# Kernel optimization log

Hardware: AMD Instinct MI355X
Metric: run time of the kernel (lower is better)

Reference implementation:

```python
import jax, jax.numpy as jnp
import numpy as np

H = 256        # hidden_dim == num_features
C = 10         # num_classes
N = 100000     # nodes
E = 1600000    # edges
BN_EPS = 1e-5
NEG_SLOPE = 0.1


def _bn(h, gamma, beta):
    # training-mode BatchNorm1d over node dim, biased variance (torch semantics)
    mu = jnp.mean(h, axis=0)
    var = jnp.mean(jnp.square(h - mu), axis=0)
    return (h - mu) * jax.lax.rsqrt(var + BN_EPS) * gamma + beta


def setup_inputs() -> dict:
    key = jax.random.key(0)
    ks = jax.random.split(key, 12)
    s = 1.0 / np.sqrt(H)
    x = jax.random.normal(ks[0], (N, H), dtype=jnp.float32)
    edge_index = jax.random.randint(ks[1], (2, E), 0, N, dtype=jnp.int64)
    return {
        "x": x,
        "edge_index": edge_index,
        # GIN MLP: lin1 -> bn -> relu -> lin2
        "W1": jax.random.uniform(ks[2], (H, H), jnp.float32, -s, s),
        "b1": jnp.zeros((H,), jnp.float32),
        "g_mlp": jnp.ones((H,), jnp.float32),
        "be_mlp": jnp.zeros((H,), jnp.float32),
        "W2": jax.random.uniform(ks[3], (H, H), jnp.float32, -s, s),
        "b2": jnp.zeros((H,), jnp.float32),
        # bn4
        "g4": jnp.ones((H,), jnp.float32),
        "be4": jnp.zeros((H,), jnp.float32),
        # head
        "Wl1": jax.random.uniform(ks[4], (H, H // 2), jnp.float32, -s, s),
        "bl1": jnp.zeros((H // 2,), jnp.float32),
        "Wl3": jax.random.uniform(ks[5], (H // 2, C), jnp.float32, -s, s),
        "bl3": jnp.zeros((C,), jnp.float32),
    }


def reference(x, edge_index, W1, b1, g_mlp, be_mlp, W2, b2, g4, be4, Wl1, bl1, Wl3, bl3):
    lrelu = lambda h: jax.nn.leaky_relu(h, NEG_SLOPE)
    src, dst = edge_index[0], edge_index[1]
    # GINConv: sum-aggregate neighbor messages (source_to_target), eps=0
    agg = jax.ops.segment_sum(x[src], dst, num_segments=x.shape[0])  # [N,H]
    h = agg + x  # (1+eps)*x + sum
    # PyG MLP([H,H,H]): lin -> batch_norm -> relu -> lin (plain last)
    h = jax.nn.relu(_bn(h @ W1 + b1, g_mlp, be_mlp)) @ W2 + b2
    x1 = lrelu(h)                     # relu(conv1(...), 0.1); dropout p=0
    h = lrelu(x1)                     # relu(x1, 0.1)
    h = lrelu(_bn(h, g4, be4))        # relu(bn4(x), 0.1); dropout p=0
    h = x + 0.01 * h                  # residual with original features
    h = lrelu(h @ Wl1 + bl1)
    return h @ Wl3 + bl3              # [N, C]
```

## Files before the change

### kernel.cpp

```cpp
#include <hip/hip_runtime.h>

constexpr int NN = 100000;
constexpr int NE = 1600000;
constexpr int NBUCK = 782;
constexpr int CGRID = 98;

typedef __attribute__((ext_vector_type(4))) float  f32x4;
typedef __attribute__((ext_vector_type(2))) float  f32x2;
typedef __attribute__((ext_vector_type(8))) short  bf16x8;

__device__ __forceinline__ float bf2f(unsigned short u) {
  union { unsigned int i; float f; } c;
  c.i = ((unsigned int)u) << 16;
  return c.f;
}
__device__ __forceinline__ short f2bf(float f) {
  union { float f; unsigned int i; } c; c.f = f;
  unsigned int i = c.i + 0x7fffu + ((c.i >> 16) & 1u);
  return (short)(i >> 16);
}
__device__ __forceinline__ unsigned char f2fp8(float f) {
  int w = __builtin_amdgcn_cvt_pk_fp8_f32(f, 0.f, 0, false);
  return (unsigned char)(w & 0xff);
}
__device__ __forceinline__ void up4(int wv, float* f) {
  f32x2 a = __builtin_amdgcn_cvt_pk_f32_fp8(wv, false);
  f32x2 b = __builtin_amdgcn_cvt_pk_f32_fp8(wv, true);
  f[0] = a[0]; f[1] = a[1]; f[2] = b[0]; f[3] = b[1];
}

__device__ __forceinline__ void gload16(const void* g, void* l) {
  __builtin_amdgcn_global_load_lds(
      (const __attribute__((address_space(1))) unsigned int*)g,
      (__attribute__((address_space(3))) unsigned int*)l, 16, 0, 0);
}

__global__ void k_detect(const int* __restrict__ ew, int* __restrict__ flag,
                         float* __restrict__ zst) {
  __shared__ int bad;
  if (threadIdx.x == 0) bad = 0;
  for (int i = threadIdx.x; i < 1024; i += 256) zst[i] = 0.f;
  __syncthreads();
  int nz = 0;
  for (int i = threadIdx.x; i < 2048; i += 256) nz |= ew[2 * i + 1];
  if (nz) atomicOr(&bad, 1);
  __syncthreads();
  if (threadIdx.x == 0) *flag = (bad == 0) ? 1 : 0;
}

__global__ void k_cvtW(const float* __restrict__ W1, const float* __restrict__ W2,
                       const float* __restrict__ Wl1, const float* __restrict__ Wl3,
                       unsigned char* __restrict__ W1T8, unsigned char* __restrict__ W2T8,
                       short* __restrict__ Wl1T, short* __restrict__ Wl3T) {
  int b = blockIdx.x, t = threadIdx.x;
  if (b < 256)       W1T8[b * 256 + t]       = f2fp8(W1[t * 256 + b]);
  else if (b < 512){ int n = b - 256; W2T8[n * 256 + t] = f2fp8(W2[t * 256 + n]); }
  else if (b < 640){ int n = b - 512; Wl1T[n * 256 + t] = f2bf(Wl1[t * 128 + n]); }
  else {
    if (t < 128) {
#pragma unroll
      for (int c = 0; c < 16; ++c)
        Wl3T[c * 128 + t] = (c < 10) ? f2bf(Wl3[t * 10 + c]) : (short)0;
    }
  }
}

__global__ void k_cvtX(const float* __restrict__ x, void* __restrict__ xq) {
  int c = blockIdx.x * 256 + threadIdx.x;
  float4 a = ((const float4*)x)[2 * (size_t)c];
  float4 b = ((const float4*)x)[2 * (size_t)c + 1];
  int p0 = 0, p1 = 0;
  p0 = __builtin_amdgcn_cvt_pk_fp8_f32(a.x, a.y, p0, false);
  p0 = __builtin_amdgcn_cvt_pk_fp8_f32(a.z, a.w, p0, true);
  p1 = __builtin_amdgcn_cvt_pk_fp8_f32(b.x, b.y, p1, false);
  p1 = __builtin_amdgcn_cvt_pk_fp8_f32(b.z, b.w, p1, true);
  ((int2*)xq)[c] = make_int2(p0, p1);
}

__global__ __launch_bounds__(1024) void k_count(const int* __restrict__ ew,
                                                const int* __restrict__ flag,
                                                int* __restrict__ cntmat) {
  __shared__ int lcnt[NBUCK];
  int m64 = *flag;
  int t = threadIdx.x;
  for (int i = t; i < NBUCK; i += 1024) lcnt[i] = 0;
  __syncthreads();
  int base = blockIdx.x * 16384;
#pragma unroll
  for (int u = 0; u < 16; u++) {
    int e = base + u * 1024 + t;
    if (e < NE) {
      int d = m64 ? ew[2 * (NE + e)] : ew[NE + e];
      atomicAdd(&lcnt[d >> 7], 1);
    }
  }
  __syncthreads();
  for (int i = t; i < NBUCK; i += 1024) cntmat[blockIdx.x * NBUCK + i] = lcnt[i];
}

__global__ __launch_bounds__(1024) void k_colscan(int* __restrict__ cntmat,
                                                  int* __restrict__ bases,
                                                  int* __restrict__ off_) {
  __shared__ int tot[1024];
  int t = threadIdx.x;
  int sum = 0;
  if (t < NBUCK) {
    for (int g = 0; g < CGRID; g++) sum += cntmat[g * NBUCK + t];
    tot[t] = sum;
  }
  __syncthreads();
  int v = (t < NBUCK) ? sum : 0;
  for (int o = 1; o < 1024; o <<= 1) {
    int u = (t >= o && t < NBUCK) ? tot[t - o] : 0;
    __syncthreads();
    if (t < NBUCK) tot[t] += u;
    __syncthreads();
  }
  if (t < NBUCK) {
    int b = tot[t] - v;
    bases[t] = b;
    int run = b;
    for (int g = 0; g < CGRID; g++) {
      int c = cntmat[g * NBUCK + t];
      cntmat[g * NBUCK + t] = run;
      run += c;
    }
  }
  if (t == NBUCK) bases[NBUCK] = NE;
  if (t == NBUCK + 1) off_[NN] = NE;
}

__global__ __launch_bounds__(1024) void k_scatter(const int* __restrict__ ew,
                                                  const int* __restrict__ flag,
                                                  const int* __restrict__ cntmat,
                                                  int* __restrict__ pairs) {
  __shared__ int lcur[NBUCK];
  int m64 = *flag;
  int t = threadIdx.x;
  for (int i = t; i < NBUCK; i += 1024) lcur[i] = cntmat[blockIdx.x * NBUCK + i];
  __syncthreads();
  int base = blockIdx.x * 16384;
#pragma unroll
  for (int u = 0; u < 16; u++) {
    int e = base + u * 1024 + t;
    if (e < NE) {
      int d = m64 ? ew[2 * (NE + e)] : ew[NE + e];
      int s = m64 ? ew[2 * e] : ew[e];
      int slot = atomicAdd(&lcur[d >> 7], 1);
      pairs[slot] = s | ((d & 127) << 17);
    }
  }
}

__global__ __launch_bounds__(256) void k_bsort(const int* __restrict__ pairs,
                                               const int* __restrict__ bases,
                                               int* __restrict__ off_,
                                               int* __restrict__ csr) {
  __shared__ int lcnt[128], lofs[128], lcur[128];
  int b = blockIdx.x, t = threadIdx.x;
  int s0 = bases[b], s1 = bases[b + 1];
  if (t < 128) lcnt[t] = 0;
  __syncthreads();
  for (int j = s0 + t; j < s1; j += 256) atomicAdd(&lcnt[(pairs[j] >> 17) & 127], 1);
  __syncthreads();
  int v = (t < 128) ? lcnt[t] : 0;
  if (t < 128) lofs[t] = v;
  __syncthreads();
  for (int o = 1; o < 128; o <<= 1) {
    int u = (t >= o && t < 128) ? lofs[t - o] : 0;
    __syncthreads();
    if (t < 128) lofs[t] += u;
    __syncthreads();
  }
  if (t < 128) {
    int ex = lofs[t] - v;
    lcur[t] = ex;
    int node = b * 128 + t;
    if (node < NN) off_[node] = s0 + ex;
  }
  __syncthreads();
  for (int j = s0 + t; j < s1; j += 256) {
    int p = pairs[j];
    int slot = atomicAdd(&lcur[(p >> 17) & 127], 1);
    csr[s0 + slot] = p & 0x1FFFF;
  }
}

__global__ __launch_bounds__(256) void k_agg2(const void* __restrict__ xq,
                                              const int* __restrict__ off_,
                                              const int* __restrict__ csr,
                                              unsigned char* __restrict__ h0) {
  int node = blockIdx.x * 4 + (threadIdx.x >> 6);
  int lane = threadIdx.x & 63;
  const unsigned char* xb = (const unsigned char*)xq;
  size_t boff = (size_t)lane * 4;
  int s0 = off_[node], s1 = off_[node + 1];
  int sw = *(const int*)(xb + (size_t)node * 256 + boff);
  f32x2 slo = __builtin_amdgcn_cvt_pk_f32_fp8(sw, false);
  f32x2 shi = __builtin_amdgcn_cvt_pk_f32_fp8(sw, true);
  float a0 = slo[0], a1 = slo[1], a2 = shi[0], a3 = shi[1];
  int j = s0;
  while (j + 8 <= s1) {
    int idx[8];
#pragma unroll
    for (int u = 0; u < 8; u++) idx[u] = csr[j + u];
    int w[8];
#pragma unroll
    for (int u = 0; u < 8; u++) w[u] = *(const int*)(xb + (size_t)idx[u] * 256 + boff);
#pragma unroll
    for (int u = 0; u < 8; u++) {
      f32x2 lo = __builtin_amdgcn_cvt_pk_f32_fp8(w[u], false);
      f32x2 hi = __builtin_amdgcn_cvt_pk_f32_fp8(w[u], true);
      a0 += lo[0]; a1 += lo[1]; a2 += hi[0]; a3 += hi[1];
    }
    j += 8;
  }
  if (j + 4 <= s1) {
    int idx[4];
#pragma unroll
    for (int u = 0; u < 4; u++) idx[u] = csr[j + u];
    int w[4];
#pragma unroll
    for (int u = 0; u < 4; u++) w[u] = *(const int*)(xb + (size_t)idx[u] * 256 + boff);
#pragma unroll
    for (int u = 0; u < 4; u++) {
      f32x2 lo = __builtin_amdgcn_cvt_pk_f32_fp8(w[u], false);
      f32x2 hi = __builtin_amdgcn_cvt_pk_f32_fp8(w[u], true);
      a0 += lo[0]; a1 += lo[1]; a2 += hi[0]; a3 += hi[1];
    }
    j += 4;
  }
  for (; j < s1; j++) {
    int s = csr[j];
    int w = *(const int*)(xb + (size_t)s * 256 + boff);
    f32x2 lo = __builtin_amdgcn_cvt_pk_f32_fp8(w, false);
    f32x2 hi = __builtin_amdgcn_cvt_pk_f32_fp8(w, true);
    a0 += lo[0]; a1 += lo[1]; a2 += hi[0]; a3 += hi[1];
  }
  int o = 0;
  o = __builtin_amdgcn_cvt_pk_fp8_f32(a0, a1, o, false);
  o = __builtin_amdgcn_cvt_pk_fp8_f32(a2, a3, o, true);
  ((int*)h0)[(size_t)node * 64 + lane] = o;
}

template <int ACT, int TIN, int STATS>
__global__ __launch_bounds__(256, 2) void k_gemm8(
    const unsigned char* __restrict__ A, const unsigned char* __restrict__ BT,
    const float* __restrict__ bias, unsigned char* __restrict__ C, int M,
    const float* __restrict__ tsum, const float* __restrict__ tssq,
    const float* __restrict__ tg, const float* __restrict__ tbe,
    float* __restrict__ gsum, float* __restrict__ gssq) {
  __shared__ char smem[32768];
  __shared__ float lsc[256], lsh[256];
  __shared__ float lsum[128], lssq[128];
  int tid = threadIdx.x, lane = tid & 63, w = tid >> 6;
  if (TIN) {
    float mu = tsum[tid] / (float)M;
    float var = tssq[tid] / (float)M - mu * mu;
    float rs = rsqrtf(var + 1e-5f);
    float sc = tg[tid] * rs;
    lsc[tid] = sc; lsh[tid] = tbe[tid] - mu * sc;
  }
  if (STATS && tid < 128) { lsum[tid] = 0.f; lssq[tid] = 0.f; }
  int bm = blockIdx.x >> 1, bn = blockIdx.x & 1;
  int bm0 = bm * 128, bn0 = bn * 128;
  int wm = w >> 1, wn = w & 1;
  int lr = lane & 15, lg = lane >> 4;
  f32x4 acc[4][4] = {};
  __syncthreads();

  int4 stg[2];

#pragma unroll 1
  for (int it = 0; it < 4; ++it) {
    int b = it & 1;
    if (it == 0) {
      if (TIN) {
#pragma unroll
        for (int i = 0; i < 2; ++i) {
          int p = i * 256 + tid, unit = p >> 3, u = (p & 7) ^ (unit & 7);
          int srow = unit * 2 + (u >> 2), slot = u & 3;
          int grow = bm0 + srow; if (grow > M - 1) grow = M - 1;
          stg[i] = *(const int4*)(A + (size_t)grow * 256 + slot * 16);
        }
      } else {
#pragma unroll
        for (int q = 0; q < 2; ++q) {
          int wc = w * 2 + q;
          int p = wc * 64 + lane, unit = p >> 3, u = (p & 7) ^ (unit & 7);
          int srow = unit * 2 + (u >> 2), slot = u & 3;
          int grow = bm0 + srow; if (grow > M - 1) grow = M - 1;
          gload16(A + (size_t)grow * 256 + slot * 16, smem + wc * 1024);
        }
      }
#pragma unroll
      for (int q = 0; q < 2; ++q) {
        int wc = w * 2 + q;
        int p = wc * 64 + lane, unit = p >> 3, u = (p & 7) ^ (unit & 7);
        int srow = unit * 2 + (u >> 2), slot = u & 3;
        gload16(BT + (size_t)(bn0 + srow) * 256 + slot * 16, smem + 8192 + wc * 1024);
      }
      if (TIN) {
#pragma unroll
        for (int i = 0; i < 2; ++i) {
          int p = i * 256 + tid, unit = p >> 3, u = (p & 7) ^ (unit & 7);
          int slot = u & 3;
          int k0 = slot * 16;
          float f[16];
          up4(stg[i].x, f); up4(stg[i].y, f + 4); up4(stg[i].z, f + 8); up4(stg[i].w, f + 12);
#pragma unroll
          for (int jj = 0; jj < 16; ++jj) f[jj] = fmaxf(f[jj] * lsc[k0 + jj] + lsh[k0 + jj], 0.f);
          int w0 = 0, w1 = 0, w2 = 0, w3 = 0;
          w0 = __builtin_amdgcn_cvt_pk_fp8_f32(f[0], f[1], w0, false);
          w0 = __builtin_amdgcn_cvt_pk_fp8_f32(f[2], f[3], w0, true);
          w1 = __builtin_amdgcn_cvt_pk_fp8_f32(f[4], f[5], w1, false);
          w1 = __builtin_amdgcn_cvt_pk_fp8_f32(f[6], f[7], w1, true);
          w2 = __builtin_amdgcn_cvt_pk_fp8_f32(f[8], f[9], w2, false);
          w2 = __builtin_amdgcn_cvt_pk_fp8_f32(f[10], f[11], w2, true);
          w3 = __builtin_amdgcn_cvt_pk_fp8_f32(f[12], f[13], w3, false);
          w3 = __builtin_amdgcn_cvt_pk_fp8_f32(f[14], f[15], w3, true);
          *(int4*)(smem + p * 16) = make_int4(w0, w1, w2, w3);
        }
      }
      __syncthreads();
    }
    int ktn = (it + 1) * 64;
    if (it < 3) {
      char* nb = smem + (b ^ 1) * 16384;
      if (TIN) {
#pragma unroll
        for (int i = 0; i < 2; ++i) {
          int p = i * 256 + tid, unit = p >> 3, u = (p & 7) ^ (unit & 7);
          int srow = unit * 2 + (u >> 2), slot = u & 3;
          int grow = bm0 + srow; if (grow > M - 1) grow = M - 1;
          stg[i] = *(const int4*)(A + (size_t)grow * 256 + ktn + slot * 16);
        }
      } else {
#pragma unroll
        for (int q = 0; q < 2; ++q) {
          int wc = w * 2 + q;
          int p = wc * 64 + lane, unit = p >> 3, u = (p & 7) ^ (unit & 7);
          int srow = unit * 2 + (u >> 2), slot = u & 3;
          int grow = bm0 + srow; if (grow > M - 1) grow = M - 1;
          gload16(A + (size_t)grow * 256 + ktn + slot * 16, nb + wc * 1024);
        }
      }
#pragma unroll
      for (int q = 0; q < 2; ++q) {
        int wc = w * 2 + q;
        int p = wc * 64 + lane, unit = p >> 3, u = (p & 7) ^ (unit & 7);
        int srow = unit * 2 + (u >> 2), slot = u & 3;
        gload16(BT + (size_t)(bn0 + srow) * 256 + ktn + slot * 16, nb + 8192 + wc * 1024);
      }
    }
    const char* sa = smem + b * 16384;
    const char* sb = sa + 8192;
#pragma unroll
    for (int ks = 0; ks < 2; ++ks) {
      long af[4], bfr[4];
#pragma unroll
      for (int mi = 0; mi < 4; ++mi) {
        int row = wm * 64 + mi * 16 + lr;
        int unit = row >> 1;
        int u = ((row & 1) * 4 + ks * 2 + (lg >> 1)) ^ (unit & 7);
        af[mi] = *(const long*)(sa + unit * 128 + u * 16 + (lg & 1) * 8);
      }
#pragma unroll
      for (int ni = 0; ni < 4; ++ni) {
        int row = wn * 64 + ni * 16 + lr;
        int unit = row >> 1;
        int u = ((row & 1) * 4 + ks * 2 + (lg >> 1)) ^ (unit & 7);
        bfr[ni] = *(const long*)(sb + unit * 128 + u * 16 + (lg & 1) * 8);
      }
#pragma unroll
      for (int mi = 0; mi < 4; ++mi)
#pragma unroll
        for (int ni = 0; ni < 4; ++ni)
          acc[mi][ni] = __builtin_amdgcn_mfma_f32_16x16x32_fp8_fp8(af[mi], bfr[ni], acc[mi][ni], 0, 0, 0);
    }
    if (TIN && it < 3) {
      char* nb = smem + (b ^ 1) * 16384;
#pragma unroll
      for (int i = 0; i < 2; ++i) {
        int p = i * 256 + tid, unit = p >> 3, u = (p & 7) ^ (unit & 7);
        int slot = u & 3;
        int k0 = ktn + slot * 16;
        float f[16];
        up4(stg[i].x, f); up4(stg[i].y, f + 4); up4(stg[i].z, f + 8); up4(stg[i].w, f + 12);
#pragma unroll
        for (int jj = 0; jj < 16; ++jj) f[jj] = fmaxf(f[jj] * lsc[k0 + jj] + lsh[k0 + jj], 0.f);
        int w0 = 0, w1 = 0, w2 = 0, w3 = 0;
        w0 = __builtin_amdgcn_cvt_pk_fp8_f32(f[0], f[1], w0, false);
        w0 = __builtin_amdgcn_cvt_pk_fp8_f32(f[2], f[3], w0, true);
        w1 = __builtin_amdgcn_cvt_pk_fp8_f32(f[4], f[5], w1, false);
        w1 = __builtin_amdgcn_cvt_pk_fp8_f32(f[6], f[7], w1, true);
        w2 = __builtin_amdgcn_cvt_pk_fp8_f32(f[8], f[9], w2, false);
        w2 = __builtin_amdgcn_cvt_pk_fp8_f32(f[10], f[11], w2, true);
        w3 = __builtin_amdgcn_cvt_pk_fp8_f32(f[12], f[13], w3, false);
        w3 = __builtin_amdgcn_cvt_pk_fp8_f32(f[14], f[15], w3, true);
        *(int4*)(nb + p * 16) = make_int4(w0, w1, w2, w3);
      }
    }
    __syncthreads();
  }

  unsigned char* zs = (unsigned char*)smem;
#pragma unroll
  for (int ni = 0; ni < 4; ++ni) {
    int col = wn * 64 + ni * 16 + lr;
    float bv = bias[bn0 + col];
    float ps = 0.f, pq = 0.f;
#pragma unroll
    for (int mi = 0; mi < 4; ++mi) {
#pragma unroll
      for (int r = 0; r < 4; ++r) {
        int row = wm * 64 + mi * 16 + lg * 4 + r;
        float tv = acc[mi][ni][r] + bv;
        if (ACT == 1) tv = tv > 0.f ? tv : 0.01f * tv;
        if (STATS && (bm0 + row) < M) { ps += tv; pq += tv * tv; }
        zs[row * 144 + col] = f2fp8(tv);
      }
    }
    if (STATS) {
      ps += __shfl_xor(ps, 16); pq += __shfl_xor(pq, 16);
      ps += __shfl_xor(ps, 32); pq += __shfl_xor(pq, 32);
      if (lane < 16) {
        atomicAdd(&lsum[wn * 64 + ni * 16 + lane], ps);
        atomicAdd(&lssq[wn * 64 + ni * 16 + lane], pq);
      }
    }
  }
  __syncthreads();
  {
    int row = tid >> 1;
    int grow = bm0 + row;
    if (grow < M) {
#pragma unroll
      for (int i = 0; i < 4; ++i) {
        int cs = (tid & 1) * 64 + i * 16;
        int4 v = *(const int4*)(zs + row * 144 + cs);
        *(int4*)(C + (size_t)grow * 256 + bn0 + cs) = v;
      }
    }
  }
  if (STATS) {
    if (tid < 128) {
      atomicAdd(&gsum[bn0 + tid], lsum[tid]);
      atomicAdd(&gssq[bn0 + tid], lssq[tid]);
    }
  }
}

__global__ __launch_bounds__(256, 2) void k_head(const unsigned char* __restrict__ Vq,
                                                 const float* __restrict__ x,
                                                 const short* __restrict__ BT,
                                                 const float* __restrict__ bl1,
                                                 const short* __restrict__ wl3t,
                                                 const float* __restrict__ bl3,
                                                 const float* __restrict__ tsum,
                                                 const float* __restrict__ tssq,
                                                 const float* __restrict__ tg,
                                                 const float* __restrict__ tbe,
                                                 float* __restrict__ out, int M) {
  __shared__ char smem[65536];
  __shared__ float lsc[256], lsh[256];
  __shared__ short wl3s[2048];
  int tid = threadIdx.x;
  int lane = tid & 63, w = tid >> 6;
  {
    float mu = tsum[tid] / (float)M;
    float var = tssq[tid] / (float)M - mu * mu;
    float rs = rsqrtf(var + 1e-5f);
    float sc = tg[tid] * rs;
    lsc[tid] = sc; lsh[tid] = tbe[tid] - mu * sc;
  }
  {
    int p = w * 64 + lane;
    gload16(wl3t + (size_t)p * 8, (char*)wl3s + w * 1024);
  }
  int bm0 = blockIdx.x * 128;
  int wm = w >> 1, wn = w & 1;
  int lr = lane & 15, lg = lane >> 4;
  f32x4 acc[4][4] = {};
  __syncthreads();

  int2 stgv[4];
  float stgx[4][8];

#pragma unroll 1
  for (int it = 0; it < 4; ++it) {
    int b = it & 1;
    if (it == 0) {
#pragma unroll
      for (int i = 0; i < 4; ++i) {
        int p = tid + 256 * i, row = p >> 3, s = (p & 7) ^ (row & 7);
        int grow = bm0 + row; if (grow > M - 1) grow = M - 1;
        size_t base = (size_t)grow * 256 + s * 8;
        stgv[i] = *(const int2*)(Vq + base);
        *(float4*)&stgx[i][0] = *(const float4*)(x + base);
        *(float4*)&stgx[i][4] = *(const float4*)(x + base + 4);
      }
#pragma unroll
      for (int q = 0; q < 4; ++q) {
        int wc = w * 4 + q;
        int p = wc * 64 + lane, row = p >> 3, s = (p & 7) ^ (row & 7);
        gload16(BT + (size_t)row * 256 + s * 8, smem + 16384 + wc * 1024);
      }
#pragma unroll
      for (int i = 0; i < 4; ++i) {
        int p = tid + 256 * i, row = p >> 3, s = (p & 7) ^ (row & 7);
        int k0 = s * 8;
        float fv[8];
        up4(stgv[i].x, fv); up4(stgv[i].y, fv + 4);
        bf16x8 o;
#pragma unroll
        for (int jj = 0; jj < 8; ++jj) {
          float f = fv[jj] * lsc[k0 + jj] + lsh[k0 + jj];
          f = f > 0.f ? f : 0.1f * f;
          o[jj] = f2bf(stgx[i][jj] + 0.01f * f);
        }
        *(bf16x8*)(smem + p * 16) = o;
      }
      __syncthreads();
    }
    int ktn = (it + 1) * 64;
    if (it < 3) {
      char* nb = smem + (b ^ 1) * 32768;
#pragma unroll
      for (int i = 0; i < 4; ++i) {
        int p = tid + 256 * i, row = p >> 3, s = (p & 7) ^ (row & 7);
        int grow = bm0 + row; if (grow > M - 1) grow = M - 1;
        size_t base = (size_t)grow * 256 + ktn + s * 8;
        stgv[i] = *(const int2*)(Vq + base);
        *(float4*)&stgx[i][0] = *(const float4*)(x + base);
        *(float4*)&stgx[i][4] = *(const float4*)(x + base + 4);
      }
#pragma unroll
      for (int q = 0; q < 4; ++q) {
        int wc = w * 4 + q;
        int p = wc * 64 + lane, row = p >> 3, s = (p & 7) ^ (row & 7);
        gload16(BT + (size_t)row * 256 + ktn + s * 8, nb + 16384 + wc * 1024);
      }
    }
    const char* sa = smem + b * 32768;
    const char* sb = sa + 16384;
#pragma unroll
    for (int ks = 0; ks < 2; ++ks) {
      bf16x8 af[4], bfr[4];
#pragma unroll
      for (int mi = 0; mi < 4; ++mi) {
        int row = wm * 64 + mi * 16 + lr;
        int q = (lg + 4 * ks) ^ (row & 7);
        af[mi] = *(const bf16x8*)(sa + row * 128 + q * 16);
      }
#pragma unroll
      for (int ni = 0; ni < 4; ++ni) {
        int row = wn * 64 + ni * 16 + lr;
        int q = (lg + 4 * ks) ^ (row & 7);
        bfr[ni] = *(const bf16x8*)(sb + row * 128 + q * 16);
      }
#pragma unroll
      for (int mi = 0; mi < 4; ++mi)
#pragma unroll
        for (int ni = 0; ni < 4; ++ni)
          acc[mi][ni] = __builtin_amdgcn_mfma_f32_16x16x32_bf16(af[mi], bfr[ni], acc[mi][ni], 0, 0, 0);
    }
    if (it < 3) {
      char* nb = smem + (b ^ 1) * 32768;
#pragma unroll
      for (int i = 0; i < 4; ++i) {
        int p = tid + 256 * i, row = p >> 3, s = (p & 7) ^ (row & 7);
        int k0 = ktn + s * 8;
        float fv[8];
        up4(stgv[i].x, fv); up4(stgv[i].y, fv + 4);
        bf16x8 o;
#pragma unroll
        for (int jj = 0; jj < 8; ++jj) {
          float f = fv[jj] * lsc[k0 + jj] + lsh[k0 + jj];
          f = f > 0.f ? f : 0.1f * f;
          o[jj] = f2bf(stgx[i][jj] + 0.01f * f);
        }
        *(bf16x8*)(nb + p * 16) = o;
      }
    }
    __syncthreads();
  }

  short* zs = (short*)smem;
#pragma unroll
  for (int ni = 0; ni < 4; ++ni) {
    int col = wn * 64 + ni * 16 + lr;
    float bv = bl1[col];
#pragma unroll
    for (int mi = 0; mi < 4; ++mi) {
#pragma unroll
      for (int r = 0; r < 4; ++r) {
        int row = wm * 64 + mi * 16 + lg * 4 + r;
        float tv = acc[mi][ni][r] + bv;
        tv = tv > 0.f ? tv : 0.1f * tv;
        zs[row * 136 + col] = f2bf(tv);
      }
    }
  }
  __syncthreads();

  f32x4 acc2[2] = {};
#pragma unroll
  for (int kk = 0; kk < 4; ++kk) {
    bf16x8 bfr = *(const bf16x8*)((const char*)wl3s + lr * 256 + (kk * 4 + lg) * 16);
#pragma unroll
    for (int m = 0; m < 2; ++m) {
      int row = (w * 2 + m) * 16 + lr;
      bf16x8 af = *(const bf16x8*)((const char*)zs + row * 272 + (kk * 4 + lg) * 16);
      acc2[m] = __builtin_amdgcn_mfma_f32_16x16x32_bf16(af, bfr, acc2[m], 0, 0, 0);
    }
  }
  if (lr < 10) {
    float bv = bl3[lr];
#pragma unroll
    for (int m = 0; m < 2; ++m) {
#pragma unroll
      for (int r = 0; r < 4; ++r) {
        int row = (w * 2 + m) * 16 + lg * 4 + r;
        int grow = bm0 + row;
        if (grow < M) out[(size_t)grow * 10 + lr] = acc2[m][r] + bv;
      }
    }
  }
}

extern "C" void kernel_launch(void* const* d_in, const int* in_sizes, int n_in,
                              void* d_out, int out_size, void* d_ws, size_t ws_size,
                              hipStream_t stream) {
  const float* x   = (const float*)d_in[0];
  const int*   ew  = (const int*)d_in[1];
  const float* W1  = (const float*)d_in[2];
  const float* b1  = (const float*)d_in[3];
  const float* g1  = (const float*)d_in[4];
  const float* be1 = (const float*)d_in[5];
  const float* W2  = (const float*)d_in[6];
  const float* b2  = (const float*)d_in[7];
  const float* g4  = (const float*)d_in[8];
  const float* be4 = (const float*)d_in[9];
  const float* Wl1 = (const float*)d_in[10];
  const float* bl1 = (const float*)d_in[11];
  const float* Wl3 = (const float*)d_in[12];
  const float* bl3 = (const float*)d_in[13];
  float* out = (float*)d_out;

  char* ws = (char*)d_ws;
  const size_t OFF_OFF  = 0;
  const size_t OFF_BASES= 400128;
  const size_t OFF_CNT  = 800256;
  const size_t OFF_WL3T = 1106944;
  const size_t OFF_STATS= 1200384;
  const size_t OFF_FLAG = 1208576;
  const size_t OFF_W1T  = 1209216;
  const size_t OFF_W2T  = 1340288;
  const size_t OFF_WL1T = 1471360;
  const size_t OFF_CSR  = 1536896;
  const size_t OFF_BUFA = 7936896;
  const size_t OFF_BUFB = 59136896;
  if (ws_size < 110336896) return;

  int* off_  = (int*)(ws + OFF_OFF);
  int* bases_= (int*)(ws + OFF_BASES);
  int* cnt_  = (int*)(ws + OFF_CNT);
  float* sum1 = (float*)(ws + OFF_STATS);
  float* ssq1 = sum1 + 256;
  float* sum4 = sum1 + 512;
  float* ssq4 = sum1 + 768;
  int* flag_ = (int*)(ws + OFF_FLAG);
  unsigned char* W1T8 = (unsigned char*)(ws + OFF_W1T);
  unsigned char* W2T8 = (unsigned char*)(ws + OFF_W2T);
  short* Wl1T = (short*)(ws + OFF_WL1T);
  short* Wl3T = (short*)(ws + OFF_WL3T);
  int* csr_   = (int*)(ws + OFF_CSR);
  unsigned char* bufA = (unsigned char*)(ws + OFF_BUFA);
  unsigned char* bufB = (unsigned char*)(ws + OFF_BUFB);
  int* pairs_ = (int*)(ws + OFF_BUFA);
  void* xq    = (void*)bufB;

  k_detect<<<1, 256, 0, stream>>>(ew, flag_, sum1);
  k_cvtW<<<641, 256, 0, stream>>>(W1, W2, Wl1, Wl3, W1T8, W2T8, Wl1T, Wl3T);
  k_cvtX<<<12500, 256, 0, stream>>>(x, xq);
  k_count<<<CGRID, 1024, 0, stream>>>(ew, flag_, cnt_);
  k_colscan<<<1, 1024, 0, stream>>>(cnt_, bases_, off_);
  k_scatter<<<CGRID, 1024, 0, stream>>>(ew, flag_, cnt_, pairs_);
  k_bsort<<<NBUCK, 256, 0, stream>>>(pairs_, bases_, off_, csr_);
  k_agg2<<<25000, 256, 0, stream>>>(xq, off_, csr_, bufA);
  k_gemm8<0, 0, 1><<<1564, 256, 0, stream>>>(bufA, W1T8, b1, bufB, NN,
                                             nullptr, nullptr, nullptr, nullptr,
                                             sum1, ssq1);
  k_gemm8<1, 1, 1><<<1564, 256, 0, stream>>>(bufB, W2T8, b2, bufA, NN,
                                             sum1, ssq1, g1, be1, sum4, ssq4);
  k_head<<<782, 256, 0, stream>>>(bufA, x, Wl1T, bl1, Wl3T, bl3,
                                  sum4, ssq4, g4, be4, out, NN);
}
```

Measured before the change: 263.7 us.

## Slice fp8 features into 8 column planes for cache-friendly gather aggregation

```diff
diff --git a/kernel.cpp b/kernel.cpp
--- a/kernel.cpp
+++ b/kernel.cpp
@@ -4,6 +4,7 @@
 constexpr int NE = 1600000;
 constexpr int NBUCK = 782;
 constexpr int CGRID = 98;
+constexpr size_t SLSZ = (size_t)NN * 32;
 
 typedef __attribute__((ext_vector_type(4))) float  f32x4;
 typedef __attribute__((ext_vector_type(2))) float  f32x2;
@@ -65,8 +66,9 @@
   }
 }
 
-__global__ void k_cvtX(const float* __restrict__ x, void* __restrict__ xq) {
+__global__ void k_cvtX(const float* __restrict__ x, unsigned char* __restrict__ xs) {
   int c = blockIdx.x * 256 + threadIdx.x;
+  int n = c >> 5, cg = c & 31;
   float4 a = ((const float4*)x)[2 * (size_t)c];
   float4 b = ((const float4*)x)[2 * (size_t)c + 1];
   int p0 = 0, p1 = 0;
@@ -74,7 +76,8 @@
   p0 = __builtin_amdgcn_cvt_pk_fp8_f32(a.z, a.w, p0, true);
   p1 = __builtin_amdgcn_cvt_pk_fp8_f32(b.x, b.y, p1, false);
   p1 = __builtin_amdgcn_cvt_pk_fp8_f32(b.z, b.w, p1, true);
-  ((int2*)xq)[c] = make_int2(p0, p1);
+  int slice = cg >> 2;
+  *(int2*)(xs + (size_t)slice * SLSZ + (size_t)n * 32 + (cg & 3) * 8) = make_int2(p0, p1);
 }
 
 __global__ __launch_bounds__(1024) void k_count(const int* __restrict__ ew,
@@ -186,64 +189,51 @@
   }
 }
 
-__global__ __launch_bounds__(256) void k_agg2(const void* __restrict__ xq,
+__global__ __launch_bounds__(256) void k_agg3(const unsigned char* __restrict__ xs,
                                               const int* __restrict__ off_,
                                               const int* __restrict__ csr,
-                                              unsigned char* __restrict__ h0) {
-  int node = blockIdx.x * 4 + (threadIdx.x >> 6);
+                                              unsigned char* __restrict__ hs) {
+  int slice = blockIdx.x & 7;
+  int chunk = blockIdx.x >> 3;
   int lane = threadIdx.x & 63;
-  const unsigned char* xb = (const unsigned char*)xq;
-  size_t boff = (size_t)lane * 4;
+  int sub = lane >> 3, part = lane & 7;
+  int node = chunk * 32 + (threadIdx.x >> 6) * 8 + sub;
+  const unsigned char* xb = xs + (size_t)slice * SLSZ;
+  size_t po = (size_t)part * 4;
   int s0 = off_[node], s1 = off_[node + 1];
-  int sw = *(const int*)(xb + (size_t)node * 256 + boff);
+  int sw = *(const int*)(xb + (size_t)node * 32 + po);
   f32x2 slo = __builtin_amdgcn_cvt_pk_f32_fp8(sw, false);
   f32x2 shi = __builtin_amdgcn_cvt_pk_f32_fp8(sw, true);
   float a0 = slo[0], a1 = slo[1], a2 = shi[0], a3 = shi[1];
-  int j = s0;
-  while (j + 8 <= s1) {
+  for (int j = s0; j < s1; j += 8) {
     int idx[8];
-#pragma unroll
-    for (int u = 0; u < 8; u++) idx[u] = csr[j + u];
-    int w[8];
-#pragma unroll
-    for (int u = 0; u < 8; u++) w[u] = *(const int*)(xb + (size_t)idx[u] * 256 + boff);
-#pragma unroll
-    for (int u = 0; u < 8; u++) {
-      f32x2 lo = __builtin_amdgcn_cvt_pk_f32_fp8(w[u], false);
-      f32x2 hi = __builtin_amdgcn_cvt_pk_f32_fp8(w[u], true);
+    idx[0] = csr[j];
+#pragma unroll
+    for (int u = 1; u < 8; ++u) idx[u] = (j + u < s1) ? csr[j + u] : idx[0];
+    int wv[8];
+#pragma unroll
+    for (int u = 0; u < 8; ++u) wv[u] = *(const int*)(xb + (size_t)idx[u] * 32 + po);
+    {
+      f32x2 lo = __builtin_amdgcn_cvt_pk_f32_fp8(wv[0], false);
+      f32x2 hi = __builtin_amdgcn_cvt_pk_f32_fp8(wv[0], true);
       a0 += lo[0]; a1 += lo[1]; a2 += hi[0]; a3 += hi[1];
     }
-    j += 8;
-  }
-  if (j + 4 <= s1) {
-    int idx[4];
-#pragma unroll
-    for (int u = 0; u < 4; u++) idx[u] = csr[j + u];
-    int w[4];
-#pragma unroll
-    for (int u = 0; u < 4; u++) w[u] = *(const int*)(xb + (size_t)idx[u] * 256 + boff);
-#pragma unroll
-    for (int u = 0; u < 4; u++) {
-      f32x2 lo = __builtin_amdgcn_cvt_pk_f32_fp8(w[u], false);
-      f32x2 hi = __builtin_amdgcn_cvt_pk_f32_fp8(w[u], true);
-      a0 += lo[0]; a1 += lo[1]; a2 += hi[0]; a3 += hi[1];
-    }
-    j += 4;
-  }
-  for (; j < s1; j++) {
-    int s = csr[j];
-    int w = *(const int*)(xb + (size_t)s * 256 + boff);
-    f32x2 lo = __builtin_amdgcn_cvt_pk_f32_fp8(w, false);
-    f32x2 hi = __builtin_amdgcn_cvt_pk_f32_fp8(w, true);
-    a0 += lo[0]; a1 += lo[1]; a2 += hi[0]; a3 += hi[1];
+#pragma unroll
+    for (int u = 1; u < 8; ++u) {
+      if (j + u < s1) {
+        f32x2 lo = __builtin_amdgcn_cvt_pk_f32_fp8(wv[u], false);
+        f32x2 hi = __builtin_amdgcn_cvt_pk_f32_fp8(wv[u], true);
+        a0 += lo[0]; a1 += lo[1]; a2 += hi[0]; a3 += hi[1];
+      }
+    }
   }
   int o = 0;
   o = __builtin_amdgcn_cvt_pk_fp8_f32(a0, a1, o, false);
   o = __builtin_amdgcn_cvt_pk_fp8_f32(a2, a3, o, true);
-  ((int*)h0)[(size_t)node * 64 + lane] = o;
-}
-
-template <int ACT, int TIN, int STATS>
+  *(int*)(hs + (size_t)slice * SLSZ + (size_t)node * 32 + po) = o;
+}
+
+template <int ACT, int TIN, int STATS, int SLICED>
 __global__ __launch_bounds__(256, 2) void k_gemm8(
     const unsigned char* __restrict__ A, const unsigned char* __restrict__ BT,
     const float* __restrict__ bias, unsigned char* __restrict__ C, int M,
@@ -290,7 +280,13 @@
           int p = wc * 64 + lane, unit = p >> 3, u = (p & 7) ^ (unit & 7);
           int srow = unit * 2 + (u >> 2), slot = u & 3;
           int grow = bm0 + srow; if (grow > M - 1) grow = M - 1;
-          gload16(A + (size_t)grow * 256 + slot * 16, smem + wc * 1024);
+          if (SLICED) {
+            int kb = slot * 16;
+            gload16(A + (size_t)(kb >> 5) * SLSZ + (size_t)grow * 32 + (kb & 31),
+                    smem + wc * 1024);
+          } else {
+            gload16(A + (size_t)grow * 256 + slot * 16, smem + wc * 1024);
+          }
         }
       }
 #pragma unroll
@@ -342,7 +338,13 @@
           int p = wc * 64 + lane, unit = p >> 3, u = (p & 7) ^ (unit & 7);
           int srow = unit * 2 + (u >> 2), slot = u & 3;
           int grow = bm0 + srow; if (grow > M - 1) grow = M - 1;
-          gload16(A + (size_t)grow * 256 + ktn + slot * 16, nb + wc * 1024);
+          if (SLICED) {
+            int kb = ktn + slot * 16;
+            gload16(A + (size_t)(kb >> 5) * SLSZ + (size_t)grow * 32 + (kb & 31),
+                    nb + wc * 1024);
+          } else {
+            gload16(A + (size_t)grow * 256 + ktn + slot * 16, nb + wc * 1024);
+          }
         }
       }
 #pragma unroll
@@ -679,21 +681,21 @@
   unsigned char* bufA = (unsigned char*)(ws + OFF_BUFA);
   unsigned char* bufB = (unsigned char*)(ws + OFF_BUFB);
   int* pairs_ = (int*)(ws + OFF_BUFA);
-  void* xq    = (void*)bufB;
+  unsigned char* xs = bufB;
 
   k_detect<<<1, 256, 0, stream>>>(ew, flag_, sum1);
   k_cvtW<<<641, 256, 0, stream>>>(W1, W2, Wl1, Wl3, W1T8, W2T8, Wl1T, Wl3T);
-  k_cvtX<<<12500, 256, 0, stream>>>(x, xq);
+  k_cvtX<<<12500, 256, 0, stream>>>(x, xs);
   k_count<<<CGRID, 1024, 0, stream>>>(ew, flag_, cnt_);
   k_colscan<<<1, 1024, 0, stream>>>(cnt_, bases_, off_);
   k_scatter<<<CGRID, 1024, 0, stream>>>(ew, flag_, cnt_, pairs_);
   k_bsort<<<NBUCK, 256, 0, stream>>>(pairs_, bases_, off_, csr_);
-  k_agg2<<<25000, 256, 0, stream>>>(xq, off_, csr_, bufA);
-  k_gemm8<0, 0, 1><<<1564, 256, 0, stream>>>(bufA, W1T8, b1, bufB, NN,
-                                             nullptr, nullptr, nullptr, nullptr,
-                                             sum1, ssq1);
-  k_gemm8<1, 1, 1><<<1564, 256, 0, stream>>>(bufB, W2T8, b2, bufA, NN,
-                                             sum1, ssq1, g1, be1, sum4, ssq4);
+  k_agg3<<<25000, 256, 0, stream>>>(xs, off_, csr_, bufA);
+  k_gemm8<0, 0, 1, 1><<<1564, 256, 0, stream>>>(bufA, W1T8, b1, bufB, NN,
+                                                nullptr, nullptr, nullptr, nullptr,
+                                                sum1, ssq1);
+  k_gemm8<1, 1, 1, 0><<<1564, 256, 0, stream>>>(bufB, W2T8, b2, bufA, NN,
+                                                sum1, ssq1, g1, be1, sum4, ssq4);
   k_head<<<782, 256, 0, stream>>>(bufA, x, Wl1T, bl1, Wl3T, bl3,
                                   sum4, ssq4, g4, be4, out, NN);
 }
```

Result: slower. 286.9 us (+8.8%).
